# Kernel tuning notes

Hardware: AMD Instinct MI355X
Metric: run time of the kernel (lower is better)

Reference implementation:

```python
import jax, jax.numpy as jnp
import numpy as np

B, IN, OUT, K = 2048, 1024, 1024, 20


def setup_inputs() -> dict:
    key = jax.random.key(0)
    k1, k2 = jax.random.split(key)
    x = jax.random.normal(k1, (B, IN), dtype=jnp.float32)
    # per-output, per-input spline coefficients: (out_features, in_features, num_knots)
    W = jax.random.normal(k2, (OUT, IN, K), dtype=jnp.float32) * 0.1
    # evenly spaced knot grid on [-2, 2] (linspace)
    knots = jnp.linspace(-2.0, 2.0, K, dtype=jnp.float32)
    return {"x": x, "W": W, "knots": knots}


def reference(x, W, knots):
    # RBF spline basis shared across all output features (this is the fusion
    # the original per-output Python loop misses):
    # basis[b, i, k] = exp(-0.5 * ((x[b, i] - knots[k]) / h)^2)
    h = knots[1] - knots[0]  # uniform knot spacing -> RBF bandwidth
    basis = jnp.exp(-0.5 * jnp.square((x[:, :, None] - knots) / h))  # (B, IN, K)
    # Each SplineLayer o computes sum_{i,k} W[o,i,k] * basis[b,i,k]; the
    # KANBlock concatenates the OUT scalars -> a single einsum.
    return jnp.einsum("bik,oik->bo", basis, W)  # (B, OUT)
```

## Files before the change

### kernel.cpp

```cpp
#include <hip/hip_runtime.h>

#define B_DIM 2048
#define IN_DIM 1024
#define OUT_DIM 1024
#define K_KNOTS 20
#define KR (IN_DIM * K_KNOTS)
#define OUT_ELEMS (B_DIM * OUT_DIM)
#define KS 8

typedef __bf16 bf16x8 __attribute__((ext_vector_type(8)));
typedef float  f32x4  __attribute__((ext_vector_type(4)));

#define MFMA16(a, b, c) __builtin_amdgcn_mfma_f32_16x16x32_bf16(a, b, c, 0, 0, 0)

__device__ __forceinline__ unsigned short f2bf(float f) {
    unsigned int u = __float_as_uint(f);
    unsigned int r = u + 0x7fffu + ((u >> 16) & 1u);
    return (unsigned short)(r >> 16);
}

__device__ __forceinline__ unsigned int pack2(float lo, float hi) {
    return (unsigned int)f2bf(lo) | ((unsigned int)f2bf(hi) << 16);
}

__device__ __forceinline__ uint4 basis8(const float* __restrict__ x,
                                        int row, int cb,
                                        float t0k, float h, float invh) {
    const int i0  = cb / K_KNOTS;
    const int kk0 = cb - i0 * K_KNOTS;
    const int i1  = i0 + (i0 < IN_DIM - 1 ? 1 : 0);
    const float xv0 = x[(size_t)row * IN_DIM + i0];
    const float xv1 = x[(size_t)row * IN_DIM + i1];
    float v[8];
#pragma unroll
    for (int j = 0; j < 8; ++j) {
        const int kk   = kk0 + j;
        const bool cr  = kk >= K_KNOTS;
        const float xv = cr ? xv1 : xv0;
        const float kf = (float)(cr ? kk - K_KNOTS : kk);
        const float tt = __builtin_fmaf(kf, h, t0k);
        const float d  = (xv - tt) * invh;
        v[j] = __expf(-0.5f * d * d);
    }
    uint4 o;
    o.x = pack2(v[0], v[1]); o.y = pack2(v[2], v[3]);
    o.z = pack2(v[4], v[5]); o.w = pack2(v[6], v[7]);
    return o;
}

#define AOFF(s, h) (((s) * 2 + (h)) * 8192)
#define BOFF(s, h) (32768 + ((s) * 2 + (h)) * 8192)

template <int S>
__device__ __forceinline__ void tile_step_f(
        int t, int ntiles,
        const float* __restrict__ x,
        const float* __restrict__ Wf,
        unsigned short* lds,
        f32x4 (&acc)[8][4],
        int m0, int n0, int k0,
        int wave, int lane, int wm, int wn, int r15, int c0, int c1,
        int srow8, int scol,
        float t0k, float h, float invh) {
    const int aB   = S * 16384 + (wm * 128 + r15) * 64;
    const int bB   = 32768 + S * 16384 + (wn * 64 + r15) * 64;
    const int kb1  = k0 + (t + 1) * 64;
    const bool st  = (t + 1 < ntiles);
    const int cbn  = kb1 + scol;
    const int ldsw = wave * 1024 + lane * 8;

    bf16x8 a0[4], a1[4], b0[4], b1[4], s0[4], s1[4];

#pragma unroll
    for (int i = 0; i < 4; ++i) a0[i] = *(const bf16x8*)&lds[aB + i * 1024 + c0];
#pragma unroll
    for (int j = 0; j < 4; ++j) b0[j] = *(const bf16x8*)&lds[bB + j * 1024 + c0];
    __builtin_amdgcn_s_barrier();
    asm volatile("s_waitcnt lgkmcnt(0)" ::: "memory");
    __builtin_amdgcn_sched_barrier(0);
    __builtin_amdgcn_s_setprio(1);
#pragma unroll
    for (int i = 0; i < 4; ++i)
#pragma unroll
        for (int j = 0; j < 4; ++j)
            acc[i][j] = MFMA16(a0[i], b0[j], acc[i][j]);
    __builtin_amdgcn_s_setprio(0);

#pragma unroll
    for (int i = 0; i < 4; ++i) a1[i] = *(const bf16x8*)&lds[aB + i * 1024 + c1];
#pragma unroll
    for (int j = 0; j < 4; ++j) b1[j] = *(const bf16x8*)&lds[bB + j * 1024 + c1];
    __builtin_amdgcn_s_barrier();
    asm volatile("s_waitcnt lgkmcnt(0)" ::: "memory");
    __builtin_amdgcn_sched_barrier(0);
    __builtin_amdgcn_s_setprio(1);
#pragma unroll
    for (int i = 0; i < 4; ++i)
#pragma unroll
        for (int j = 0; j < 4; ++j)
            acc[i][j] = MFMA16(a1[i], b1[j], acc[i][j]);
    __builtin_amdgcn_s_setprio(0);

#pragma unroll
    for (int i = 0; i < 4; ++i) s0[i] = *(const bf16x8*)&lds[aB + (4 + i) * 1024 + c0];
    __builtin_amdgcn_s_barrier();
    asm volatile("s_waitcnt lgkmcnt(0)" ::: "memory");
    __builtin_amdgcn_sched_barrier(0);
    __builtin_amdgcn_s_setprio(1);
#pragma unroll
    for (int i = 0; i < 4; ++i)
#pragma unroll
        for (int j = 0; j < 4; ++j)
            acc[4 + i][j] = MFMA16(s0[i], b0[j], acc[4 + i][j]);
    __builtin_amdgcn_s_setprio(0);

    f32x4 wA0, wA1, wB0, wB1, wC0, wC1, wD0, wD1;
    if (st) {
        const float* g0 = Wf + (size_t)(n0 + wave * 16 + srow8) * KR + cbn;
        const float* g1 = g0 + (size_t)8 * KR;
        const float* g2 = g0 + (size_t)128 * KR;
        const float* g3 = g0 + (size_t)136 * KR;
        wA0 = *(const f32x4*)g0;       wA1 = *(const f32x4*)(g0 + 4);
        wB0 = *(const f32x4*)g1;       wB1 = *(const f32x4*)(g1 + 4);
        wC0 = *(const f32x4*)g2;       wC1 = *(const f32x4*)(g2 + 4);
        wD0 = *(const f32x4*)g3;       wD1 = *(const f32x4*)(g3 + 4);
        const int ra = m0 + wave * 16 + srow8;
        uint4 d0 = basis8(x, ra,       cbn, t0k, h, invh);
        uint4 d1 = basis8(x, ra + 8,   cbn, t0k, h, invh);
        uint4 d2 = basis8(x, ra + 128, cbn, t0k, h, invh);
        uint4 d3 = basis8(x, ra + 136, cbn, t0k, h, invh);
        *(uint4*)&lds[AOFF(S ^ 1, 0) + ldsw]       = d0;
        *(uint4*)&lds[AOFF(S ^ 1, 0) + 512 + ldsw] = d1;
        *(uint4*)&lds[AOFF(S ^ 1, 1) + ldsw]       = d2;
        *(uint4*)&lds[AOFF(S ^ 1, 1) + 512 + ldsw] = d3;
    }

#pragma unroll
    for (int i = 0; i < 4; ++i) s1[i] = *(const bf16x8*)&lds[aB + (4 + i) * 1024 + c1];
    __builtin_amdgcn_s_barrier();
    asm volatile("s_waitcnt lgkmcnt(0)" ::: "memory");
    __builtin_amdgcn_sched_barrier(0);
    __builtin_amdgcn_s_setprio(1);
#pragma unroll
    for (int i = 0; i < 4; ++i)
#pragma unroll
        for (int j = 0; j < 4; ++j)
            acc[4 + i][j] = MFMA16(s1[i], b1[j], acc[4 + i][j]);
    __builtin_amdgcn_s_setprio(0);

    if (st) {
        uint4 o0 = make_uint4(pack2(wA0[0], wA0[1]), pack2(wA0[2], wA0[3]),
                              pack2(wA1[0], wA1[1]), pack2(wA1[2], wA1[3]));
        uint4 o1 = make_uint4(pack2(wB0[0], wB0[1]), pack2(wB0[2], wB0[3]),
                              pack2(wB1[0], wB1[1]), pack2(wB1[2], wB1[3]));
        uint4 o2 = make_uint4(pack2(wC0[0], wC0[1]), pack2(wC0[2], wC0[3]),
                              pack2(wC1[0], wC1[1]), pack2(wC1[2], wC1[3]));
        uint4 o3 = make_uint4(pack2(wD0[0], wD0[1]), pack2(wD0[2], wD0[3]),
                              pack2(wD1[0], wD1[1]), pack2(wD1[2], wD1[3]));
        *(uint4*)&lds[BOFF(S ^ 1, 0) + ldsw]       = o0;
        *(uint4*)&lds[BOFF(S ^ 1, 0) + 512 + ldsw] = o1;
        *(uint4*)&lds[BOFF(S ^ 1, 1) + ldsw]       = o2;
        *(uint4*)&lds[BOFF(S ^ 1, 1) + 512 + ldsw] = o3;
    }

    asm volatile("s_waitcnt lgkmcnt(0)" ::: "memory");
    __builtin_amdgcn_s_barrier();
}

__global__ void __launch_bounds__(512, 2)
kan_gemmf(const float* __restrict__ x,
          const float* __restrict__ Wf,
          const float* __restrict__ knots,
          float* __restrict__ part) {
    __shared__ __align__(16) unsigned short lds[65536];

    constexpr int KPBk   = KR / KS;
    constexpr int NTILES = KPBk / 64;

    const int id  = blockIdx.x;
    const int z   = id & 7;
    const int ord = id >> 3;
    const int mt  = ord & 7;
    const int nt  = ord >> 3;
    const int m0  = mt * 256;
    const int n0  = nt * 256;
    const int k0  = z * KPBk;

    const int tid  = threadIdx.x;
    const int wave = tid >> 6;
    const int lane = tid & 63;
    const int wm   = wave >> 2;
    const int wn   = wave & 3;

    const int srow8 = lane >> 3;
    const int scol  = ((lane & 7) ^ srow8) * 8;

    const float t0k  = knots[0];
    const float h    = knots[1] - t0k;
    const float invh = 1.0f / h;

    f32x4 acc[8][4];
#pragma unroll
    for (int i = 0; i < 8; ++i)
#pragma unroll
        for (int j = 0; j < 4; ++j) acc[i][j] = (f32x4){0.f, 0.f, 0.f, 0.f};

    const int q   = lane >> 4;
    const int r15 = lane & 15;
    const int r7  = lane & 7;
    const int c0  = (q ^ r7) * 8;
    const int c1  = ((4 + q) ^ r7) * 8;

    {
        const int cb0  = k0 + scol;
        const int ldsw = wave * 1024 + lane * 8;
        const int ra   = m0 + wave * 16 + srow8;
        uint4 d0 = basis8(x, ra,       cb0, t0k, h, invh);
        uint4 d1 = basis8(x, ra + 8,   cb0, t0k, h, invh);
        uint4 d2 = basis8(x, ra + 128, cb0, t0k, h, invh);
        uint4 d3 = basis8(x, ra + 136, cb0, t0k, h, invh);
        *(uint4*)&lds[AOFF(0, 0) + ldsw]       = d0;
        *(uint4*)&lds[AOFF(0, 0) + 512 + ldsw] = d1;
        *(uint4*)&lds[AOFF(0, 1) + ldsw]       = d2;
        *(uint4*)&lds[AOFF(0, 1) + 512 + ldsw] = d3;
        const float* g0 = Wf + (size_t)(n0 + wave * 16 + srow8) * KR + cb0;
        const float* g1 = g0 + (size_t)8 * KR;
        const float* g2 = g0 + (size_t)128 * KR;
        const float* g3 = g0 + (size_t)136 * KR;
        f32x4 wA0 = *(const f32x4*)g0, wA1 = *(const f32x4*)(g0 + 4);
        f32x4 wB0 = *(const f32x4*)g1, wB1 = *(const f32x4*)(g1 + 4);
        f32x4 wC0 = *(const f32x4*)g2, wC1 = *(const f32x4*)(g2 + 4);
        f32x4 wD0 = *(const f32x4*)g3, wD1 = *(const f32x4*)(g3 + 4);
        uint4 o0 = make_uint4(pack2(wA0[0], wA0[1]), pack2(wA0[2], wA0[3]),
                              pack2(wA1[0], wA1[1]), pack2(wA1[2], wA1[3]));
        uint4 o1 = make_uint4(pack2(wB0[0], wB0[1]), pack2(wB0[2], wB0[3]),
                              pack2(wB1[0], wB1[1]), pack2(wB1[2], wB1[3]));
        uint4 o2 = make_uint4(pack2(wC0[0], wC0[1]), pack2(wC0[2], wC0[3]),
                              pack2(wC1[0], wC1[1]), pack2(wC1[2], wC1[3]));
        uint4 o3 = make_uint4(pack2(wD0[0], wD0[1]), pack2(wD0[2], wD0[3]),
                              pack2(wD1[0], wD1[1]), pack2(wD1[2], wD1[3]));
        *(uint4*)&lds[BOFF(0, 0) + ldsw]       = o0;
        *(uint4*)&lds[BOFF(0, 0) + 512 + ldsw] = o1;
        *(uint4*)&lds[BOFF(0, 1) + ldsw]       = o2;
        *(uint4*)&lds[BOFF(0, 1) + 512 + ldsw] = o3;
        asm volatile("s_waitcnt lgkmcnt(0)" ::: "memory");
        __builtin_amdgcn_s_barrier();
    }

    for (int tt = 0; tt < NTILES; tt += 2) {
        tile_step_f<0>(tt,     NTILES, x, Wf, lds, acc, m0, n0, k0,
                       wave, lane, wm, wn, r15, c0, c1, srow8, scol,
                       t0k, h, invh);
        tile_step_f<1>(tt + 1, NTILES, x, Wf, lds, acc, m0, n0, k0,
                       wave, lane, wm, wn, r15, c0, c1, srow8, scol,
                       t0k, h, invh);
    }

    float* dst = part + (size_t)z * OUT_ELEMS;
#pragma unroll
    for (int i = 0; i < 8; ++i)
#pragma unroll
        for (int j = 0; j < 4; ++j)
#pragma unroll
            for (int r = 0; r < 4; ++r) {
                const int row = m0 + wm * 128 + i * 16 + q * 4 + r;
                const int c   = n0 + wn * 64  + j * 16 + r15;
                dst[(size_t)row * OUT_DIM + c] = acc[i][j][r];
            }
}

template <int KSr>
__global__ void kan_reduce(const float* __restrict__ part, float* __restrict__ out) {
    const int idx = (blockIdx.x * 256 + threadIdx.x) * 4;
    f32x4 s = *(const f32x4*)(part + idx);
#pragma unroll
    for (int z = 1; z < KSr; ++z)
        s += *(const f32x4*)(part + (size_t)z * OUT_ELEMS + idx);
    *(f32x4*)(out + idx) = s;
}

__global__ void kan_fallback(const float* __restrict__ x,
                             const float* __restrict__ W,
                             const float* __restrict__ knots,
                             float* __restrict__ out) {
    __shared__ float basis[256 * K_KNOTS];
    const int b = blockIdx.x;
    const int o = blockIdx.y * blockDim.x + threadIdx.x;
    const float invh = 1.0f / (knots[1] - knots[0]);
    const float* w = W + (size_t)o * KR;
    float sum = 0.f;
    for (int i0 = 0; i0 < IN_DIM; i0 += 256) {
        __syncthreads();
        for (int idx = threadIdx.x; idx < 256 * K_KNOTS; idx += blockDim.x) {
            const int i = i0 + idx / K_KNOTS;
            const int k = idx % K_KNOTS;
            const float d = (x[(size_t)b * IN_DIM + i] - knots[k]) * invh;
            basis[idx] = __expf(-0.5f * d * d);
        }
        __syncthreads();
        for (int r = 0; r < 256 * K_KNOTS; ++r)
            sum += basis[r] * w[(size_t)i0 * K_KNOTS + r];
    }
    out[(size_t)b * OUT_DIM + o] = sum;
}

extern "C" void kernel_launch(void* const* d_in, const int* in_sizes, int n_in,
                              void* d_out, int out_size, void* d_ws, size_t ws_size,
                              hipStream_t stream) {
    const float* x     = (const float*)d_in[0];
    const float* W     = (const float*)d_in[1];
    const float* knots = (const float*)d_in[2];
    float* out = (float*)d_out;

    const size_t part_bytes = (size_t)KS * OUT_ELEMS * 4;
    float* part = (float*)d_ws;

    if (ws_size >= part_bytes) {
        kan_gemmf<<<dim3(256), dim3(512), 0, stream>>>(x, W, knots, part);
        kan_reduce<KS><<<dim3(OUT_ELEMS / (256 * 4)), dim3(256), 0, stream>>>(part, out);
    } else {
        kan_fallback<<<dim3(B_DIM, OUT_DIM / 256), dim3(256), 0, stream>>>(x, W, knots, out);
    }
}
```

Measured before the change: 282.0 us.

## Precompute bf16 RBF basis in a prep kernel and stream it via async LDS loads

Adds a separate kernel that computes the full RBF basis once and writes it to workspace as bf16 (2048x20480). The GEMM then pulls that matrix straight into LDS with global_load_lds instead of recomputing exp values for every N-tile. W conversion switches to the hardware v_cvt_pk_bf16_f32 instruction, and the load/MFMA phases are reordered so the global loads are issued earlier. The cost is an extra ~84MB write and read of the basis matrix plus one more launch, in exchange for removing redundant exp work repeated across the 4 N-tiles.

```diff
diff --git a/kernel.cpp b/kernel.cpp
--- a/kernel.cpp
+++ b/kernel.cpp
@@ -8,6 +8,9 @@
 #define OUT_ELEMS (B_DIM * OUT_DIM)
 #define KS 8
 
+#define NPAIRS (B_DIM * IN_DIM * 5 / 2)
+#define NB_PREP_BLK (NPAIRS / 256)
+
 typedef __bf16 bf16x8 __attribute__((ext_vector_type(8)));
 typedef float  f32x4  __attribute__((ext_vector_type(4)));
 
@@ -23,50 +26,74 @@
     return (unsigned int)f2bf(lo) | ((unsigned int)f2bf(hi) << 16);
 }
 
-__device__ __forceinline__ uint4 basis8(const float* __restrict__ x,
-                                        int row, int cb,
-                                        float t0k, float h, float invh) {
-    const int i0  = cb / K_KNOTS;
-    const int kk0 = cb - i0 * K_KNOTS;
-    const int i1  = i0 + (i0 < IN_DIM - 1 ? 1 : 0);
-    const float xv0 = x[(size_t)row * IN_DIM + i0];
-    const float xv1 = x[(size_t)row * IN_DIM + i1];
+__device__ __forceinline__ unsigned int cvtpk(float lo, float hi) {
+    unsigned int r;
+    asm("v_cvt_pk_bf16_f32 %0, %1, %2" : "=v"(r) : "v"(lo), "v"(hi));
+    return r;
+}
+
+__device__ __forceinline__ void async_load16(const void* g, void* l) {
+    __builtin_amdgcn_global_load_lds(
+        (const __attribute__((address_space(1))) void*)g,
+        (__attribute__((address_space(3))) void*)l,
+        16, 0, 0);
+}
+
+__global__ void __launch_bounds__(256) prep_kernel(
+        const float* __restrict__ x,
+        const float* __restrict__ knots,
+        uint4* __restrict__ basis_out) {
+    const unsigned int p  = blockIdx.x * 256 + threadIdx.x;
+    const unsigned int n0 = 2 * p;
+    const unsigned int q0  = n0 % 5u;
+    const unsigned int bi0 = n0 / 5u;
+    const float t0   = knots[0];
+    const float h    = knots[1] - t0;
+    const float invh = 1.0f / h;
+
+    const bool cross = (q0 == 4u);
+    const unsigned int bi1 = bi0 + (cross ? 1u : 0u);
+    const float xv0 = x[bi0];
+    const float xv1 = x[bi1];
+    const float kA = (float)(4u * q0);
+    const float kB = cross ? 0.f : kA + 4.f;
+
     float v[8];
 #pragma unroll
-    for (int j = 0; j < 8; ++j) {
-        const int kk   = kk0 + j;
-        const bool cr  = kk >= K_KNOTS;
-        const float xv = cr ? xv1 : xv0;
-        const float kf = (float)(cr ? kk - K_KNOTS : kk);
-        const float tt = __builtin_fmaf(kf, h, t0k);
-        const float d  = (xv - tt) * invh;
+    for (int j = 0; j < 4; ++j) {
+        float t = __builtin_fmaf(kA + (float)j, h, t0);
+        float d = (xv0 - t) * invh;
         v[j] = __expf(-0.5f * d * d);
+    }
+#pragma unroll
+    for (int j = 0; j < 4; ++j) {
+        float t = __builtin_fmaf(kB + (float)j, h, t0);
+        float d = (xv1 - t) * invh;
+        v[4 + j] = __expf(-0.5f * d * d);
     }
     uint4 o;
     o.x = pack2(v[0], v[1]); o.y = pack2(v[2], v[3]);
     o.z = pack2(v[4], v[5]); o.w = pack2(v[6], v[7]);
-    return o;
+    basis_out[p] = o;
 }
 
 #define AOFF(s, h) (((s) * 2 + (h)) * 8192)
 #define BOFF(s, h) (32768 + ((s) * 2 + (h)) * 8192)
 
 template <int S>
-__device__ __forceinline__ void tile_step_f(
+__device__ __forceinline__ void tile_step(
         int t, int ntiles,
-        const float* __restrict__ x,
+        const unsigned short* __restrict__ Ab,
         const float* __restrict__ Wf,
         unsigned short* lds,
         f32x4 (&acc)[8][4],
         int m0, int n0, int k0,
         int wave, int lane, int wm, int wn, int r15, int c0, int c1,
-        int srow8, int scol,
-        float t0k, float h, float invh) {
+        int srow8, int scol) {
     const int aB   = S * 16384 + (wm * 128 + r15) * 64;
     const int bB   = 32768 + S * 16384 + (wn * 64 + r15) * 64;
     const int kb1  = k0 + (t + 1) * 64;
     const bool st  = (t + 1 < ntiles);
-    const int cbn  = kb1 + scol;
     const int ldsw = wave * 1024 + lane * 8;
 
     bf16x8 a0[4], a1[4], b0[4], b1[4], s0[4], s1[4];
@@ -103,40 +130,23 @@
 
 #pragma unroll
     for (int i = 0; i < 4; ++i) s0[i] = *(const bf16x8*)&lds[aB + (4 + i) * 1024 + c0];
-    __builtin_amdgcn_s_barrier();
-    asm volatile("s_waitcnt lgkmcnt(0)" ::: "memory");
-    __builtin_amdgcn_sched_barrier(0);
-    __builtin_amdgcn_s_setprio(1);
-#pragma unroll
-    for (int i = 0; i < 4; ++i)
-#pragma unroll
-        for (int j = 0; j < 4; ++j)
-            acc[4 + i][j] = MFMA16(s0[i], b0[j], acc[4 + i][j]);
-    __builtin_amdgcn_s_setprio(0);
-
-    f32x4 wA0, wA1, wB0, wB1, wC0, wC1, wD0, wD1;
+    f32x4 w0, w1, w2, w3, w4, w5, w6, w7;
     if (st) {
-        const float* g0 = Wf + (size_t)(n0 + wave * 16 + srow8) * KR + cbn;
+        const unsigned short* ga = Ab + (size_t)(m0 + wave * 16 + srow8) * KR + kb1 + scol;
+        async_load16(ga,                   &lds[AOFF(S ^ 1, 0) + wave * 1024]);
+        async_load16(ga + (size_t)8 * KR,  &lds[AOFF(S ^ 1, 0) + wave * 1024 + 512]);
+        const unsigned short* ga1 = ga + (size_t)128 * KR;
+        async_load16(ga1,                  &lds[AOFF(S ^ 1, 1) + wave * 1024]);
+        async_load16(ga1 + (size_t)8 * KR, &lds[AOFF(S ^ 1, 1) + wave * 1024 + 512]);
+        const float* g0 = Wf + (size_t)(n0 + wave * 16 + srow8) * KR + kb1 + scol;
         const float* g1 = g0 + (size_t)8 * KR;
         const float* g2 = g0 + (size_t)128 * KR;
         const float* g3 = g0 + (size_t)136 * KR;
-        wA0 = *(const f32x4*)g0;       wA1 = *(const f32x4*)(g0 + 4);
-        wB0 = *(const f32x4*)g1;       wB1 = *(const f32x4*)(g1 + 4);
-        wC0 = *(const f32x4*)g2;       wC1 = *(const f32x4*)(g2 + 4);
-        wD0 = *(const f32x4*)g3;       wD1 = *(const f32x4*)(g3 + 4);
-        const int ra = m0 + wave * 16 + srow8;
-        uint4 d0 = basis8(x, ra,       cbn, t0k, h, invh);
-        uint4 d1 = basis8(x, ra + 8,   cbn, t0k, h, invh);
-        uint4 d2 = basis8(x, ra + 128, cbn, t0k, h, invh);
-        uint4 d3 = basis8(x, ra + 136, cbn, t0k, h, invh);
-        *(uint4*)&lds[AOFF(S ^ 1, 0) + ldsw]       = d0;
-        *(uint4*)&lds[AOFF(S ^ 1, 0) + 512 + ldsw] = d1;
-        *(uint4*)&lds[AOFF(S ^ 1, 1) + ldsw]       = d2;
-        *(uint4*)&lds[AOFF(S ^ 1, 1) + 512 + ldsw] = d3;
-    }
-
-#pragma unroll
-    for (int i = 0; i < 4; ++i) s1[i] = *(const bf16x8*)&lds[aB + (4 + i) * 1024 + c1];
+        w0 = *(const f32x4*)g0; w1 = *(const f32x4*)(g0 + 4);
+        w2 = *(const f32x4*)g1; w3 = *(const f32x4*)(g1 + 4);
+        w4 = *(const f32x4*)g2; w5 = *(const f32x4*)(g2 + 4);
+        w6 = *(const f32x4*)g3; w7 = *(const f32x4*)(g3 + 4);
+    }
     __builtin_amdgcn_s_barrier();
     asm volatile("s_waitcnt lgkmcnt(0)" ::: "memory");
     __builtin_amdgcn_sched_barrier(0);
@@ -145,32 +155,45 @@
     for (int i = 0; i < 4; ++i)
 #pragma unroll
         for (int j = 0; j < 4; ++j)
+            acc[4 + i][j] = MFMA16(s0[i], b0[j], acc[4 + i][j]);
+    __builtin_amdgcn_s_setprio(0);
+
+#pragma unroll
+    for (int i = 0; i < 4; ++i) s1[i] = *(const bf16x8*)&lds[aB + (4 + i) * 1024 + c1];
+    __builtin_amdgcn_s_barrier();
+    asm volatile("s_waitcnt lgkmcnt(0)" ::: "memory");
+    __builtin_amdgcn_sched_barrier(0);
+    __builtin_amdgcn_s_setprio(1);
+#pragma unroll
+    for (int i = 0; i < 4; ++i)
+#pragma unroll
+        for (int j = 0; j < 4; ++j)
             acc[4 + i][j] = MFMA16(s1[i], b1[j], acc[4 + i][j]);
     __builtin_amdgcn_s_setprio(0);
 
     if (st) {
-        uint4 o0 = make_uint4(pack2(wA0[0], wA0[1]), pack2(wA0[2], wA0[3]),
-                              pack2(wA1[0], wA1[1]), pack2(wA1[2], wA1[3]));
-        uint4 o1 = make_uint4(pack2(wB0[0], wB0[1]), pack2(wB0[2], wB0[3]),
-                              pack2(wB1[0], wB1[1]), pack2(wB1[2], wB1[3]));
-        uint4 o2 = make_uint4(pack2(wC0[0], wC0[1]), pack2(wC0[2], wC0[3]),
-                              pack2(wC1[0], wC1[1]), pack2(wC1[2], wC1[3]));
-        uint4 o3 = make_uint4(pack2(wD0[0], wD0[1]), pack2(wD0[2], wD0[3]),
-                              pack2(wD1[0], wD1[1]), pack2(wD1[2], wD1[3]));
+        uint4 o0 = make_uint4(cvtpk(w0[0], w0[1]), cvtpk(w0[2], w0[3]),
+                              cvtpk(w1[0], w1[1]), cvtpk(w1[2], w1[3]));
+        uint4 o1 = make_uint4(cvtpk(w2[0], w2[1]), cvtpk(w2[2], w2[3]),
+                              cvtpk(w3[0], w3[1]), cvtpk(w3[2], w3[3]));
+        uint4 o2 = make_uint4(cvtpk(w4[0], w4[1]), cvtpk(w4[2], w4[3]),
+                              cvtpk(w5[0], w5[1]), cvtpk(w5[2], w5[3]));
+        uint4 o3 = make_uint4(cvtpk(w6[0], w6[1]), cvtpk(w6[2], w6[3]),
+                              cvtpk(w7[0], w7[1]), cvtpk(w7[2], w7[3]));
         *(uint4*)&lds[BOFF(S ^ 1, 0) + ldsw]       = o0;
         *(uint4*)&lds[BOFF(S ^ 1, 0) + 512 + ldsw] = o1;
         *(uint4*)&lds[BOFF(S ^ 1, 1) + ldsw]       = o2;
         *(uint4*)&lds[BOFF(S ^ 1, 1) + 512 + ldsw] = o3;
     }
 
+    if (st) asm volatile("s_waitcnt vmcnt(0)" ::: "memory");
     asm volatile("s_waitcnt lgkmcnt(0)" ::: "memory");
     __builtin_amdgcn_s_barrier();
 }
 
 __global__ void __launch_bounds__(512, 2)
-kan_gemmf(const float* __restrict__ x,
+kan_gemm8(const unsigned short* __restrict__ Ab,
           const float* __restrict__ Wf,
-          const float* __restrict__ knots,
           float* __restrict__ part) {
     __shared__ __align__(16) unsigned short lds[65536];
 
@@ -195,10 +218,6 @@
     const int srow8 = lane >> 3;
     const int scol  = ((lane & 7) ^ srow8) * 8;
 
-    const float t0k  = knots[0];
-    const float h    = knots[1] - t0k;
-    const float invh = 1.0f / h;
-
     f32x4 acc[8][4];
 #pragma unroll
     for (int i = 0; i < 8; ++i)
@@ -212,48 +231,42 @@
     const int c1  = ((4 + q) ^ r7) * 8;
 
     {
-        const int cb0  = k0 + scol;
         const int ldsw = wave * 1024 + lane * 8;
-        const int ra   = m0 + wave * 16 + srow8;
-        uint4 d0 = basis8(x, ra,       cb0, t0k, h, invh);
-        uint4 d1 = basis8(x, ra + 8,   cb0, t0k, h, invh);
-        uint4 d2 = basis8(x, ra + 128, cb0, t0k, h, invh);
-        uint4 d3 = basis8(x, ra + 136, cb0, t0k, h, invh);
-        *(uint4*)&lds[AOFF(0, 0) + ldsw]       = d0;
-        *(uint4*)&lds[AOFF(0, 0) + 512 + ldsw] = d1;
-        *(uint4*)&lds[AOFF(0, 1) + ldsw]       = d2;
-        *(uint4*)&lds[AOFF(0, 1) + 512 + ldsw] = d3;
-        const float* g0 = Wf + (size_t)(n0 + wave * 16 + srow8) * KR + cb0;
+        const unsigned short* ga = Ab + (size_t)(m0 + wave * 16 + srow8) * KR + k0 + scol;
+        async_load16(ga,                   &lds[AOFF(0, 0) + wave * 1024]);
+        async_load16(ga + (size_t)8 * KR,  &lds[AOFF(0, 0) + wave * 1024 + 512]);
+        const unsigned short* ga1 = ga + (size_t)128 * KR;
+        async_load16(ga1,                  &lds[AOFF(0, 1) + wave * 1024]);
+        async_load16(ga1 + (size_t)8 * KR, &lds[AOFF(0, 1) + wave * 1024 + 512]);
+        const float* g0 = Wf + (size_t)(n0 + wave * 16 + srow8) * KR + k0 + scol;
         const float* g1 = g0 + (size_t)8 * KR;
         const float* g2 = g0 + (size_t)128 * KR;
         const float* g3 = g0 + (size_t)136 * KR;
-        f32x4 wA0 = *(const f32x4*)g0, wA1 = *(const f32x4*)(g0 + 4);
-        f32x4 wB0 = *(const f32x4*)g1, wB1 = *(const f32x4*)(g1 + 4);
-        f32x4 wC0 = *(const f32x4*)g2, wC1 = *(const f32x4*)(g2 + 4);
-        f32x4 wD0 = *(const f32x4*)g3, wD1 = *(const f32x4*)(g3 + 4);
-        uint4 o0 = make_uint4(pack2(wA0[0], wA0[1]), pack2(wA0[2], wA0[3]),
-                              pack2(wA1[0], wA1[1]), pack2(wA1[2], wA1[3]));
-        uint4 o1 = make_uint4(pack2(wB0[0], wB0[1]), pack2(wB0[2], wB0[3]),
-                              pack2(wB1[0], wB1[1]), pack2(wB1[2], wB1[3]));
-        uint4 o2 = make_uint4(pack2(wC0[0], wC0[1]), pack2(wC0[2], wC0[3]),
-                              pack2(wC1[0], wC1[1]), pack2(wC1[2], wC1[3]));
-        uint4 o3 = make_uint4(pack2(wD0[0], wD0[1]), pack2(wD0[2], wD0[3]),
-                              pack2(wD1[0], wD1[1]), pack2(wD1[2], wD1[3]));
+        f32x4 w0 = *(const f32x4*)g0, w1 = *(const f32x4*)(g0 + 4);
+        f32x4 w2 = *(const f32x4*)g1, w3 = *(const f32x4*)(g1 + 4);
+        f32x4 w4 = *(const f32x4*)g2, w5 = *(const f32x4*)(g2 + 4);
+        f32x4 w6 = *(const f32x4*)g3, w7 = *(const f32x4*)(g3 + 4);
+        uint4 o0 = make_uint4(cvtpk(w0[0], w0[1]), cvtpk(w0[2], w0[3]),
+                              cvtpk(w1[0], w1[1]), cvtpk(w1[2], w1[3]));
+        uint4 o1 = make_uint4(cvtpk(w2[0], w2[1]), cvtpk(w2[2], w2[3]),
+                              cvtpk(w3[0], w3[1]), cvtpk(w3[2], w3[3]));
+        uint4 o2 = make_uint4(cvtpk(w4[0], w4[1]), cvtpk(w4[2], w4[3]),
+                              cvtpk(w5[0], w5[1]), cvtpk(w5[2], w5[3]));
+        uint4 o3 = make_uint4(cvtpk(w6[0], w6[1]), cvtpk(w6[2], w6[3]),
+                              cvtpk(w7[0], w7[1]), cvtpk(w7[2], w7[3]));
         *(uint4*)&lds[BOFF(0, 0) + ldsw]       = o0;
         *(uint4*)&lds[BOFF(0, 0) + 512 + ldsw] = o1;
         *(uint4*)&lds[BOFF(0, 1) + ldsw]       = o2;
         *(uint4*)&lds[BOFF(0, 1) + 512 + ldsw] = o3;
-        asm volatile("s_waitcnt lgkmcnt(0)" ::: "memory");
+        asm volatile("s_waitcnt vmcnt(0) lgkmcnt(0)" ::: "memory");
         __builtin_amdgcn_s_barrier();
     }
 
     for (int tt = 0; tt < NTILES; tt += 2) {
-        tile_step_f<0>(tt,     NTILES, x, Wf, lds, acc, m0, n0, k0,
-                       wave, lane, wm, wn, r15, c0, c1, srow8, scol,
-                       t0k, h, invh);
-        tile_step_f<1>(tt + 1, NTILES, x, Wf, lds, acc, m0, n0, k0,
-                       wave, lane, wm, wn, r15, c0, c1, srow8, scol,
-                       t0k, h, invh);
+        tile_step<0>(tt,     NTILES, Ab, Wf, lds, acc, m0, n0, k0,
+                     wave, lane, wm, wn, r15, c0, c1, srow8, scol);
+        tile_step<1>(tt + 1, NTILES, Ab, Wf, lds, acc, m0, n0, k0,
+                     wave, lane, wm, wn, r15, c0, c1, srow8, scol);
     }
 
     float* dst = part + (size_t)z * OUT_ELEMS;
@@ -312,11 +325,16 @@
     const float* knots = (const float*)d_in[2];
     float* out = (float*)d_out;
 
-    const size_t part_bytes = (size_t)KS * OUT_ELEMS * 4;
-    float* part = (float*)d_ws;
-
-    if (ws_size >= part_bytes) {
-        kan_gemmf<<<dim3(256), dim3(512), 0, stream>>>(x, W, knots, part);
+    const size_t basis_bytes = (size_t)B_DIM * KR * 2;
+    const size_t part_bytes  = (size_t)KS * OUT_ELEMS * 4;
+
+    unsigned short* Ab = (unsigned short*)d_ws;
+    float* part = (float*)((char*)d_ws + basis_bytes);
+
+    if (ws_size >= basis_bytes + part_bytes) {
+        prep_kernel<<<dim3(NB_PREP_BLK), dim3(256), 0, stream>>>(
+            x, knots, (uint4*)Ab);
+        kan_gemm8<<<dim3(256), dim3(512), 0, stream>>>(Ab, W, part);
         kan_reduce<KS><<<dim3(OUT_ELEMS / (256 * 4)), dim3(256), 0, stream>>>(part, out);
     } else {
         kan_fallback<<<dim3(B_DIM, OUT_DIM / 256), dim3(256), 0, stream>>>(x, W, knots, out);
```

New measurement: 272.1 us. 3.5% less time.
